# Kernel optimization log

Measured on AMD Instinct MI355X. Metric: run time of the kernel, lower is better.

## Reference

```python
import jax, jax.numpy as jnp
import numpy as np

B, N, K, D = 8, 32768, 128, 64
TAU, ITERS, EPS = 1.0, 10, 1e-8


def setup_inputs() -> dict:
    key = jax.random.key(0)
    k1, k2, k3 = jax.random.split(key, 3)
    xyz = jax.random.normal(k1, (B, 3, N), dtype=jnp.float32)
    feats = jax.random.normal(k2, (B, D, N), dtype=jnp.float32)
    o_scores = jax.random.uniform(k3, (B, N), dtype=jnp.float32)
    return {"xyz": xyz, "feats": feats, "o_scores": o_scores}


def _sq_dist(x, c):
    # x: (B,N,3), c: (B,K,3) -> (B,N,K) squared euclidean distance
    x2 = jnp.sum(x * x, axis=-1, keepdims=True)          # (B,N,1)
    c2 = jnp.sum(c * c, axis=-1)[:, None, :]              # (B,1,K)
    xc = jnp.einsum('bnd,bkd->bnk', x, c)                 # (B,N,K)
    return x2 + c2 - 2.0 * xc


def _wkeans_plus(x, f, s, n_clusters, iters, tau):
    # x: (B,N,3) points, f: (B,N,D) features, s: (B,N) soft weights
    n = x.shape[1]
    # deterministic init: evenly strided points as initial centroids
    init_idx = jnp.arange(n_clusters) * (n // n_clusters)
    centers = x[:, init_idx, :]                           # (B,K,3)
    w = s[..., None]                                      # (B,N,1)
    s_sum = jnp.sum(s, axis=1, keepdims=True) + EPS       # (B,1)
    gamma = None
    denom = None
    for _ in range(iters):
        d = _sq_dist(x, centers)                          # (B,N,K)
        gamma = jax.nn.softmax(-d / tau, axis=-1) * w     # (B,N,K) weighted soft assignment
        denom = jnp.sum(gamma, axis=1) + EPS              # (B,K)
        centers = jnp.einsum('bnk,bnd->bkd', gamma, x) / denom[..., None]
    pi = jnp.sum(gamma, axis=1) / s_sum                   # (B,K) mixing weights
    node_feats = jnp.einsum('bnk,bnd->bkd', gamma, f) / denom[..., None]  # (B,K,D)
    return gamma, pi, centers, node_feats


def reference(xyz, feats, o_scores):
    x = jnp.swapaxes(xyz, -1, -2)    # (B,N,3)
    f = jnp.swapaxes(feats, -1, -2)  # (B,N,D)
    gamma, pi, node_xyz, node_feats = _wkeans_plus(x, f, o_scores, K, ITERS, TAU)
    return gamma, pi, node_xyz, node_feats
```

## Files before the change

kernel.cpp:

```cpp
#include <hip/hip_runtime.h>
#include <hip/hip_bf16.h>

typedef __attribute__((ext_vector_type(8))) short short8;
typedef __attribute__((ext_vector_type(4))) float f32x4;

#define BB 8
#define NN 32768
#define KK 128
#define DD 64
#define TAU 1.0f
#define ITERS 10
#define EPSV 1e-8f
#define JPARTS 128

#define G_SZ   ((size_t)BB * NN * KK)
#define PI_OFF (G_SZ)
#define XY_OFF (PI_OFF + (size_t)BB * KK)
#define NF_OUT (XY_OFF + (size_t)BB * KK * 3)

#define SLICE_F (BB * KK * 4)
#define SS_OFF  ((ITERS + 1) * SLICE_F)
#define HDR_F   (SS_OFF + 16)
#define PART_OFF HDR_F
#define PART_F  ((size_t)JPARTS * BB * KK * DD)
#define WS_NEED_BYTES  ((PART_OFF + PART_F) * 4)

__device__ __forceinline__ unsigned pk2(float a, float b) {
    __hip_bfloat162 h = __float22bfloat162_rn(make_float2(a, b));
    unsigned u; __builtin_memcpy(&u, &h, 4); return u;
}

__global__ __launch_bounds__(256) void prep_kernel(const float* __restrict__ xyz,
                                                   const float* __restrict__ sc,
                                                   float* __restrict__ ws) {
    int b = blockIdx.x, tid = threadIdx.x, wave = tid >> 6, lane = tid & 63;
    const float* S = sc + (size_t)b * NN;
    float sum = 0.f;
    for (int i = tid; i < NN; i += 256) sum += S[i];
    #pragma unroll
    for (int m = 1; m <= 32; m <<= 1) sum += __shfl_xor(sum, m, 64);
    __shared__ float red[4];
    if (lane == 0) red[wave] = sum;
    __syncthreads();
    if (tid == 0) ws[SS_OFF + b] = red[0] + red[1] + red[2] + red[3] + EPSV;
    if (tid < KK) {
        const float* X = xyz + (size_t)b * 3 * NN;
        int i0 = tid * (NN / KK);
        ((float4*)ws)[b * KK + tid] =
            make_float4(X[i0], X[NN + i0], X[2 * NN + i0], 1.0f);
    }
}

template <bool LAST>
__global__ __launch_bounds__(256) void assign_kernel(
    const float* __restrict__ xyz, const float* __restrict__ sc,
    const float4* __restrict__ accIn,
    float* __restrict__ accOut,
    float* __restrict__ gamma_out)
{
    __shared__ float4 cLds[KK];
    __shared__ float4 wLds[512];
    __shared__ float  accW[4][512];

    const int b = blockIdx.y, blk = blockIdx.x;
    const int tid = threadIdx.x, wave = tid >> 6, lane = tid & 63;

    const float* X = xyz + (size_t)b * 3 * NN;
    const float* S = sc + (size_t)b * NN;

    const int n = blk * 512 + tid;
    const float px0 = X[n],       py0 = X[NN + n],       pz0 = X[2 * NN + n],       ps0 = S[n];
    const float px1 = X[n + 256], py1 = X[NN + n + 256], pz1 = X[2 * NN + n + 256], ps1 = S[n + 256];

    if (tid < KK) {
        float4 a = accIn[b * KK + tid];
        float denom = a.w + EPSV;
        float cx = a.x / denom, cy = a.y / denom, cz = a.z / denom;
        cLds[tid] = make_float4(2.f * cx / TAU, 2.f * cy / TAU, 2.f * cz / TAU,
                                -(cx * cx + cy * cy + cz * cz) / TAU);
    }
    __syncthreads();

    float l0a = 0.f, l0b = 0.f, l1a = 0.f, l1b = 0.f;
    #pragma unroll 8
    for (int k = 0; k < KK; k += 2) {
        float4 ca = cLds[k], cb = cLds[k + 1];
        l0a += __expf(fmaf(px0, ca.x, fmaf(py0, ca.y, fmaf(pz0, ca.z, ca.w))));
        l1a += __expf(fmaf(px1, ca.x, fmaf(py1, ca.y, fmaf(pz1, ca.z, ca.w))));
        l0b += __expf(fmaf(px0, cb.x, fmaf(py0, cb.y, fmaf(pz0, cb.z, cb.w))));
        l1b += __expf(fmaf(px1, cb.x, fmaf(py1, cb.y, fmaf(pz1, cb.z, cb.w))));
    }
    wLds[tid]       = make_float4(px0, py0, pz0, ps0 / (l0a + l0b));
    wLds[tid + 256] = make_float4(px1, py1, pz1, ps1 / (l1a + l1b));
    __syncthreads();

    const float4 c0 = cLds[lane];
    const float4 c1 = cLds[lane + 64];
    float ax0 = 0, ay0 = 0, az0 = 0, aw0 = 0;
    float ax1 = 0, ay1 = 0, az1 = 0, aw1 = 0;
    float* grow = gamma_out + ((size_t)b * NN + blk * 512 + (wave << 7)) * KK + lane;

    #pragma unroll 4
    for (int j = 0; j < 128; ++j) {
        float4 P = wLds[(wave << 7) | j];
        float g0 = __expf(fmaf(P.x, c0.x, fmaf(P.y, c0.y, fmaf(P.z, c0.z, c0.w)))) * P.w;
        float g1 = __expf(fmaf(P.x, c1.x, fmaf(P.y, c1.y, fmaf(P.z, c1.z, c1.w)))) * P.w;
        if (LAST) {
            grow[(size_t)j * KK] = g0;
            grow[(size_t)j * KK + 64] = g1;
        }
        ax0 = fmaf(g0, P.x, ax0); ay0 = fmaf(g0, P.y, ay0);
        az0 = fmaf(g0, P.z, az0); aw0 += g0;
        ax1 = fmaf(g1, P.x, ax1); ay1 = fmaf(g1, P.y, ay1);
        az1 = fmaf(g1, P.z, az1); aw1 += g1;
    }

    ((float4*)accW[wave])[lane]      = make_float4(ax0, ay0, az0, aw0);
    ((float4*)accW[wave])[lane + 64] = make_float4(ax1, ay1, az1, aw1);
    __syncthreads();
    float v0 = accW[0][tid]       + accW[1][tid]       + accW[2][tid]       + accW[3][tid];
    float v1 = accW[0][tid + 256] + accW[1][tid + 256] + accW[2][tid + 256] + accW[3][tid + 256];
    float* ag = accOut + b * (KK * 4);
    atomicAdd(ag + tid, v0);
    atomicAdd(ag + tid + 256, v1);
}

__global__ void final_kernel(const float* __restrict__ ws, float* __restrict__ out) {
    int b = blockIdx.x, k = threadIdx.x;
    float4 a = ((const float4*)(ws + ITERS * SLICE_F))[b * KK + k];
    float denom = a.w + EPSV;
    float* oxyz = out + XY_OFF + (size_t)(b * KK + k) * 3;
    oxyz[0] = a.x / denom; oxyz[1] = a.y / denom; oxyz[2] = a.z / denom;
    out[PI_OFF + b * KK + k] = a.w / ws[SS_OFF + b];
}

__global__ __launch_bounds__(256) void nf_mfma2(const float* __restrict__ gamma,
                                                const float* __restrict__ feats,
                                                float* __restrict__ dst) {
    __shared__ unsigned short gT[KK * 40];
    const int b = blockIdx.y, part = blockIdx.x;
    const int tid = threadIdx.x, wave = tid >> 6, lane = tid & 63;
    const int r = lane & 15, hi = lane >> 4;
    const int p = tid & 15, q0 = tid >> 4;

    f32x4 acc[2][4];
    #pragma unroll
    for (int kt = 0; kt < 2; kt++)
        #pragma unroll
        for (int dt = 0; dt < 4; dt++) acc[kt][dt] = (f32x4){0.f, 0.f, 0.f, 0.f};

    const float* gb = gamma + (size_t)b * NN * KK + (size_t)part * 256 * KK;
    const float* fb = feats + (size_t)b * DD * NN;
    const int n0 = part * 256;

    for (int ch = 0; ch < 8; ++ch) {
        const float* gr0 = gb + (size_t)(ch * 32 + 2 * p) * KK;
        const float* gr1 = gr0 + KK;
        unsigned* rowd = (unsigned*)gT;
        #pragma unroll
        for (int s = 0; s < 2; ++s) {
            int q = q0 + 16 * s;
            float4 x = *(const float4*)(gr0 + 4 * q);
            float4 y = *(const float4*)(gr1 + 4 * q);
            rowd[(4 * q + 0) * 20 + p] = pk2(x.x, y.x);
            rowd[(4 * q + 1) * 20 + p] = pk2(x.y, y.y);
            rowd[(4 * q + 2) * 20 + p] = pk2(x.z, y.z);
            rowd[(4 * q + 3) * 20 + p] = pk2(x.w, y.w);
        }
        __syncthreads();

        const unsigned short* a0p = gT + (wave * 32 + r) * 40 + hi * 8;
        short8 a0 = *(const short8*)a0p;
        short8 a1 = *(const short8*)(a0p + 16 * 40);
        const int nn = n0 + ch * 32 + hi * 8;
        #pragma unroll
        for (int dt = 0; dt < 4; ++dt) {
            const float* fr = fb + (size_t)(dt * 16 + r) * NN + nn;
            float4 x = *(const float4*)fr;
            float4 y = *(const float4*)(fr + 4);
            union { unsigned u[4]; short8 s; } bu;
            bu.u[0] = pk2(x.x, x.y); bu.u[1] = pk2(x.z, x.w);
            bu.u[2] = pk2(y.x, y.y); bu.u[3] = pk2(y.z, y.w);
            acc[0][dt] = __builtin_amdgcn_mfma_f32_16x16x32_bf16(a0, bu.s, acc[0][dt], 0, 0, 0);
            acc[1][dt] = __builtin_amdgcn_mfma_f32_16x16x32_bf16(a1, bu.s, acc[1][dt], 0, 0, 0);
        }
        __syncthreads();
    }

    float* pdst = dst + ((size_t)(b * JPARTS + part)) * (KK * DD) + (size_t)(wave * 32) * DD;
    #pragma unroll
    for (int kt = 0; kt < 2; kt++)
        #pragma unroll
        for (int dt = 0; dt < 4; dt++)
            #pragma unroll
            for (int rr = 0; rr < 4; rr++)
                pdst[(kt * 16 + hi * 4 + rr) * DD + dt * 16 + r] = acc[kt][dt][rr];
}

__global__ __launch_bounds__(256) void nf_compute_atomic(const float* __restrict__ gamma,
                                                         const float* __restrict__ feats,
                                                         float* __restrict__ dst) {
    __shared__ float gLds[32 * 128];
    __shared__ float fLds[64 * 33];
    const int b = blockIdx.y, part = blockIdx.x, tid = threadIdx.x;
    const int kq = (tid & 15) * 8, dg = (tid >> 4) * 4;
    float acc[8][4];
    #pragma unroll
    for (int i = 0; i < 8; i++)
        #pragma unroll
        for (int u = 0; u < 4; u++) acc[i][u] = 0.f;
    const float* gb = gamma + (size_t)b * NN * KK + (size_t)part * (NN / JPARTS) * KK;
    const float* fb = feats + (size_t)b * DD * NN + part * (NN / JPARTS);
    for (int ch = 0; ch < (NN / JPARTS) / 32; ++ch) {
        const float4* gs = (const float4*)(gb + (size_t)ch * 32 * KK);
        #pragma unroll
        for (int i = 0; i < 4; i++) ((float4*)gLds)[tid + i * 256] = gs[tid + i * 256];
        #pragma unroll
        for (int i = 0; i < 2; i++) {
            int idx = tid + i * 256;
            int d = idx >> 3, c4 = (idx & 7) * 4;
            float4 fv = *(const float4*)(fb + (size_t)d * NN + ch * 32 + c4);
            float* fr = &fLds[d * 33 + c4];
            fr[0] = fv.x; fr[1] = fv.y; fr[2] = fv.z; fr[3] = fv.w;
        }
        __syncthreads();
        #pragma unroll 4
        for (int nl = 0; nl < 32; ++nl) {
            float4 g0 = *(const float4*)&gLds[nl * 128 + kq];
            float4 g1 = *(const float4*)&gLds[nl * 128 + kq + 4];
            float fv[4];
            #pragma unroll
            for (int u = 0; u < 4; u++) fv[u] = fLds[(dg + u) * 33 + nl];
            float gk[8] = {g0.x, g0.y, g0.z, g0.w, g1.x, g1.y, g1.z, g1.w};
            #pragma unroll
            for (int i = 0; i < 8; i++)
                #pragma unroll
                for (int u = 0; u < 4; u++)
                    acc[i][u] = fmaf(gk[i], fv[u], acc[i][u]);
        }
        __syncthreads();
    }
    float* nf = dst + (size_t)b * KK * DD;
    #pragma unroll
    for (int i = 0; i < 8; i++)
        #pragma unroll
        for (int u = 0; u < 4; u++)
            atomicAdd(&nf[(kq + i) * DD + dg + u], acc[i][u]);
}

__global__ __launch_bounds__(256) void nf_reduce(const float* __restrict__ ws,
                                                 float* __restrict__ out) {
    int idx = blockIdx.x * 256 + threadIdx.x;
    int b = idx >> 13, e = idx & 8191;
    const float* p = ws + PART_OFF + (size_t)b * JPARTS * (KK * DD) + e;
    float sum = 0.f;
    #pragma unroll 8
    for (int j = 0; j < JPARTS; ++j) sum += p[(size_t)j * (KK * DD)];
    int k = e >> 6;
    float denom = ws[ITERS * SLICE_F + (b * KK + k) * 4 + 3] + EPSV;
    out[NF_OUT + idx] = sum / denom;
}

__global__ __launch_bounds__(256) void nf_finalize(const float* __restrict__ ws,
                                                   float* __restrict__ out) {
    int idx = blockIdx.x * 256 + threadIdx.x;
    int bk = idx / DD;
    float denom = ws[ITERS * SLICE_F + bk * 4 + 3] + EPSV;
    out[NF_OUT + idx] = out[NF_OUT + idx] / denom;
}

extern "C" void kernel_launch(void* const* d_in, const int* in_sizes, int n_in,
                              void* d_out, int out_size, void* d_ws, size_t ws_size,
                              hipStream_t stream) {
    const float* xyz = (const float*)d_in[0];
    const float* feats = (const float*)d_in[1];
    const float* sc = (const float*)d_in[2];
    float* out = (float*)d_out;
    float* ws = (float*)d_ws;

    hipMemsetAsync(ws, 0, (size_t)HDR_F * sizeof(float), stream);
    prep_kernel<<<BB, 256, 0, stream>>>(xyz, sc, ws);

    for (int it = 0; it < ITERS - 1; it++) {
        assign_kernel<false><<<dim3(64, BB), 256, 0, stream>>>(
            xyz, sc, (const float4*)(ws + it * SLICE_F),
            ws + (it + 1) * SLICE_F, out);
    }
    assign_kernel<true><<<dim3(64, BB), 256, 0, stream>>>(
        xyz, sc, (const float4*)(ws + (ITERS - 1) * SLICE_F),
        ws + ITERS * SLICE_F, out);

    final_kernel<<<BB, KK, 0, stream>>>(ws, out);

    if (ws_size >= WS_NEED_BYTES) {
        nf_mfma2<<<dim3(JPARTS, BB), 256, 0, stream>>>(out, feats, ws + PART_OFF);
        nf_reduce<<<256, 256, 0, stream>>>(ws, out);
    } else {
        hipMemsetAsync(out + NF_OUT, 0, (size_t)BB * KK * DD * sizeof(float), stream);
        nf_compute_atomic<<<dim3(JPARTS, BB), 256, 0, stream>>>(out, feats, out + NF_OUT);
        nf_finalize<<<256, 256, 0, stream>>>(ws, out);
    }
}
```

Measured before the change: 294.9 us.

## Fuse softmax normalizer into assignment loop via DPP wave reduction

Drops the separate per-point pass that computed the softmax denominator with 128 exponentials per point. The exponentials already computed in the main per-cluster loop are now summed across the wave with a DPP reduction plus readlane, and each value is scaled by the score divided by that sum. Centroids are now held in registers per lane rather than staged through LDS. This roughly halves the exp work, but adds a serial cross-lane reduction chain inside every point iteration.

```diff
diff --git a/kernel.cpp b/kernel.cpp
--- a/kernel.cpp
+++ b/kernel.cpp
@@ -28,6 +28,23 @@
 __device__ __forceinline__ unsigned pk2(float a, float b) {
     __hip_bfloat162 h = __float22bfloat162_rn(make_float2(a, b));
     unsigned u; __builtin_memcpy(&u, &h, 4); return u;
+}
+__device__ __forceinline__ float rdl(float v, int l) {
+    return __int_as_float(__builtin_amdgcn_readlane(__float_as_int(v), l));
+}
+template <int CTRL, int RMASK>
+__device__ __forceinline__ float dpp_add(float x) {
+    int t = __builtin_amdgcn_update_dpp(0, __float_as_int(x), CTRL, RMASK, 0xf, false);
+    return x + __int_as_float(t);
+}
+__device__ __forceinline__ float wave_sum64(float x) {
+    x = dpp_add<0x111, 0xf>(x);
+    x = dpp_add<0x112, 0xf>(x);
+    x = dpp_add<0x114, 0xf>(x);
+    x = dpp_add<0x118, 0xf>(x);
+    x = dpp_add<0x142, 0xa>(x);
+    x = dpp_add<0x143, 0xc>(x);
+    return rdl(x, 63);
 }
 
 __global__ __launch_bounds__(256) void prep_kernel(const float* __restrict__ xyz,
@@ -58,7 +75,6 @@
     float* __restrict__ accOut,
     float* __restrict__ gamma_out)
 {
-    __shared__ float4 cLds[KK];
     __shared__ float4 wLds[512];
     __shared__ float  accW[4][512];
 
@@ -69,33 +85,20 @@
     const float* S = sc + (size_t)b * NN;
 
     const int n = blk * 512 + tid;
-    const float px0 = X[n],       py0 = X[NN + n],       pz0 = X[2 * NN + n],       ps0 = S[n];
-    const float px1 = X[n + 256], py1 = X[NN + n + 256], pz1 = X[2 * NN + n + 256], ps1 = S[n + 256];
-
-    if (tid < KK) {
-        float4 a = accIn[b * KK + tid];
-        float denom = a.w + EPSV;
-        float cx = a.x / denom, cy = a.y / denom, cz = a.z / denom;
-        cLds[tid] = make_float4(2.f * cx / TAU, 2.f * cy / TAU, 2.f * cz / TAU,
-                                -(cx * cx + cy * cy + cz * cz) / TAU);
-    }
+    wLds[tid]       = make_float4(X[n], X[NN + n], X[2 * NN + n], S[n]);
+    wLds[tid + 256] = make_float4(X[n + 256], X[NN + n + 256], X[2 * NN + n + 256], S[n + 256]);
+
+    float4 a0 = accIn[b * KK + lane];
+    float4 a1 = accIn[b * KK + 64 + lane];
+    float d0 = a0.w + EPSV, d1 = a1.w + EPSV;
+    float cx0 = a0.x / d0, cy0 = a0.y / d0, cz0 = a0.z / d0;
+    float cx1 = a1.x / d1, cy1 = a1.y / d1, cz1 = a1.z / d1;
+    const float4 c0 = make_float4(2.f * cx0 / TAU, 2.f * cy0 / TAU, 2.f * cz0 / TAU,
+                                  -(cx0 * cx0 + cy0 * cy0 + cz0 * cz0) / TAU);
+    const float4 c1 = make_float4(2.f * cx1 / TAU, 2.f * cy1 / TAU, 2.f * cz1 / TAU,
+                                  -(cx1 * cx1 + cy1 * cy1 + cz1 * cz1) / TAU);
     __syncthreads();
 
-    float l0a = 0.f, l0b = 0.f, l1a = 0.f, l1b = 0.f;
-    #pragma unroll 8
-    for (int k = 0; k < KK; k += 2) {
-        float4 ca = cLds[k], cb = cLds[k + 1];
-        l0a += __expf(fmaf(px0, ca.x, fmaf(py0, ca.y, fmaf(pz0, ca.z, ca.w))));
-        l1a += __expf(fmaf(px1, ca.x, fmaf(py1, ca.y, fmaf(pz1, ca.z, ca.w))));
-        l0b += __expf(fmaf(px0, cb.x, fmaf(py0, cb.y, fmaf(pz0, cb.z, cb.w))));
-        l1b += __expf(fmaf(px1, cb.x, fmaf(py1, cb.y, fmaf(pz1, cb.z, cb.w))));
-    }
-    wLds[tid]       = make_float4(px0, py0, pz0, ps0 / (l0a + l0b));
-    wLds[tid + 256] = make_float4(px1, py1, pz1, ps1 / (l1a + l1b));
-    __syncthreads();
-
-    const float4 c0 = cLds[lane];
-    const float4 c1 = cLds[lane + 64];
     float ax0 = 0, ay0 = 0, az0 = 0, aw0 = 0;
     float ax1 = 0, ay1 = 0, az1 = 0, aw1 = 0;
     float* grow = gamma_out + ((size_t)b * NN + blk * 512 + (wave << 7)) * KK + lane;
@@ -103,8 +106,11 @@
     #pragma unroll 4
     for (int j = 0; j < 128; ++j) {
         float4 P = wLds[(wave << 7) | j];
-        float g0 = __expf(fmaf(P.x, c0.x, fmaf(P.y, c0.y, fmaf(P.z, c0.z, c0.w)))) * P.w;
-        float g1 = __expf(fmaf(P.x, c1.x, fmaf(P.y, c1.y, fmaf(P.z, c1.z, c1.w)))) * P.w;
+        float e0 = __expf(fmaf(P.x, c0.x, fmaf(P.y, c0.y, fmaf(P.z, c0.z, c0.w))));
+        float e1 = __expf(fmaf(P.x, c1.x, fmaf(P.y, c1.y, fmaf(P.z, c1.z, c1.w))));
+        float l = wave_sum64(e0 + e1);
+        float w = __fdividef(P.w, l);
+        float g0 = e0 * w, g1 = e1 * w;
         if (LAST) {
             grow[(size_t)j * KK] = g0;
             grow[(size_t)j * KK + 64] = g1;
```

After: 322.9 us. +9.5%, slower.

## Fold prep into first assign and final kernels, atomically reduce MFMA node features

Applied to the files above, without the earlier changes.

Removes the separate prep kernel by computing initial centroids inside the first assign launch and moving the score-sum reduction into the final kernel. The MFMA node-feature kernel now atomically adds its partial tiles straight into the output, replacing the per-part workspace partials and the separate reduce pass with a memset plus a light finalize. This cuts launches and the large partial-buffer write and read, at the cost of heavy float atomic contention on a small output.

```diff
diff --git a/kernel.cpp b/kernel.cpp
--- a/kernel.cpp
+++ b/kernel.cpp
@@ -19,39 +19,14 @@
 #define NF_OUT (XY_OFF + (size_t)BB * KK * 3)
 
 #define SLICE_F (BB * KK * 4)
-#define SS_OFF  ((ITERS + 1) * SLICE_F)
-#define HDR_F   (SS_OFF + 16)
-#define PART_OFF HDR_F
-#define PART_F  ((size_t)JPARTS * BB * KK * DD)
-#define WS_NEED_BYTES  ((PART_OFF + PART_F) * 4)
+#define HDR_F   ((ITERS + 1) * SLICE_F)
 
 __device__ __forceinline__ unsigned pk2(float a, float b) {
     __hip_bfloat162 h = __float22bfloat162_rn(make_float2(a, b));
     unsigned u; __builtin_memcpy(&u, &h, 4); return u;
 }
 
-__global__ __launch_bounds__(256) void prep_kernel(const float* __restrict__ xyz,
-                                                   const float* __restrict__ sc,
-                                                   float* __restrict__ ws) {
-    int b = blockIdx.x, tid = threadIdx.x, wave = tid >> 6, lane = tid & 63;
-    const float* S = sc + (size_t)b * NN;
-    float sum = 0.f;
-    for (int i = tid; i < NN; i += 256) sum += S[i];
-    #pragma unroll
-    for (int m = 1; m <= 32; m <<= 1) sum += __shfl_xor(sum, m, 64);
-    __shared__ float red[4];
-    if (lane == 0) red[wave] = sum;
-    __syncthreads();
-    if (tid == 0) ws[SS_OFF + b] = red[0] + red[1] + red[2] + red[3] + EPSV;
-    if (tid < KK) {
-        const float* X = xyz + (size_t)b * 3 * NN;
-        int i0 = tid * (NN / KK);
-        ((float4*)ws)[b * KK + tid] =
-            make_float4(X[i0], X[NN + i0], X[2 * NN + i0], 1.0f);
-    }
-}
-
-template <bool LAST>
+template <bool FIRST, bool LAST>
 __global__ __launch_bounds__(256) void assign_kernel(
     const float* __restrict__ xyz, const float* __restrict__ sc,
     const float4* __restrict__ accIn,
@@ -73,9 +48,15 @@
     const float px1 = X[n + 256], py1 = X[NN + n + 256], pz1 = X[2 * NN + n + 256], ps1 = S[n + 256];
 
     if (tid < KK) {
-        float4 a = accIn[b * KK + tid];
-        float denom = a.w + EPSV;
-        float cx = a.x / denom, cy = a.y / denom, cz = a.z / denom;
+        float cx, cy, cz;
+        if (FIRST) {
+            int i0 = tid * (NN / KK);
+            cx = X[i0]; cy = X[NN + i0]; cz = X[2 * NN + i0];
+        } else {
+            float4 a = accIn[b * KK + tid];
+            float denom = a.w + EPSV;
+            cx = a.x / denom; cy = a.y / denom; cz = a.z / denom;
+        }
         cLds[tid] = make_float4(2.f * cx / TAU, 2.f * cy / TAU, 2.f * cz / TAU,
                                 -(cx * cx + cy * cy + cz * cz) / TAU);
     }
@@ -125,18 +106,31 @@
     atomicAdd(ag + tid + 256, v1);
 }
 
-__global__ void final_kernel(const float* __restrict__ ws, float* __restrict__ out) {
-    int b = blockIdx.x, k = threadIdx.x;
-    float4 a = ((const float4*)(ws + ITERS * SLICE_F))[b * KK + k];
-    float denom = a.w + EPSV;
-    float* oxyz = out + XY_OFF + (size_t)(b * KK + k) * 3;
-    oxyz[0] = a.x / denom; oxyz[1] = a.y / denom; oxyz[2] = a.z / denom;
-    out[PI_OFF + b * KK + k] = a.w / ws[SS_OFF + b];
+__global__ __launch_bounds__(256) void final_kernel(const float* __restrict__ sc,
+                                                    const float* __restrict__ ws,
+                                                    float* __restrict__ out) {
+    int b = blockIdx.x, tid = threadIdx.x, wave = tid >> 6, lane = tid & 63;
+    const float* S = sc + (size_t)b * NN;
+    float sum = 0.f;
+    for (int i = tid; i < NN; i += 256) sum += S[i];
+    #pragma unroll
+    for (int m = 1; m <= 32; m <<= 1) sum += __shfl_xor(sum, m, 64);
+    __shared__ float red[4];
+    if (lane == 0) red[wave] = sum;
+    __syncthreads();
+    if (tid < KK) {
+        float ssum = red[0] + red[1] + red[2] + red[3] + EPSV;
+        float4 a = ((const float4*)(ws + ITERS * SLICE_F))[b * KK + tid];
+        float denom = a.w + EPSV;
+        float* oxyz = out + XY_OFF + (size_t)(b * KK + tid) * 3;
+        oxyz[0] = a.x / denom; oxyz[1] = a.y / denom; oxyz[2] = a.z / denom;
+        out[PI_OFF + b * KK + tid] = a.w / ssum;
+    }
 }
 
 __global__ __launch_bounds__(256) void nf_mfma2(const float* __restrict__ gamma,
                                                 const float* __restrict__ feats,
-                                                float* __restrict__ dst) {
+                                                float* __restrict__ nf_acc) {
     __shared__ unsigned short gT[KK * 40];
     const int b = blockIdx.y, part = blockIdx.x;
     const int tid = threadIdx.x, wave = tid >> 6, lane = tid & 63;
@@ -187,78 +181,15 @@
         __syncthreads();
     }
 
-    float* pdst = dst + ((size_t)(b * JPARTS + part)) * (KK * DD) + (size_t)(wave * 32) * DD;
+    float* nf = nf_acc + (size_t)b * KK * DD + (size_t)(wave * 32) * DD;
     #pragma unroll
     for (int kt = 0; kt < 2; kt++)
         #pragma unroll
         for (int dt = 0; dt < 4; dt++)
             #pragma unroll
             for (int rr = 0; rr < 4; rr++)
-                pdst[(kt * 16 + hi * 4 + rr) * DD + dt * 16 + r] = acc[kt][dt][rr];
-}
-
-__global__ __launch_bounds__(256) void nf_compute_atomic(const float* __restrict__ gamma,
-                                                         const float* __restrict__ feats,
-                                                         float* __restrict__ dst) {
-    __shared__ float gLds[32 * 128];
-    __shared__ float fLds[64 * 33];
-    const int b = blockIdx.y, part = blockIdx.x, tid = threadIdx.x;
-    const int kq = (tid & 15) * 8, dg = (tid >> 4) * 4;
-    float acc[8][4];
-    #pragma unroll
-    for (int i = 0; i < 8; i++)
-        #pragma unroll
-        for (int u = 0; u < 4; u++) acc[i][u] = 0.f;
-    const float* gb = gamma + (size_t)b * NN * KK + (size_t)part * (NN / JPARTS) * KK;
-    const float* fb = feats + (size_t)b * DD * NN + part * (NN / JPARTS);
-    for (int ch = 0; ch < (NN / JPARTS) / 32; ++ch) {
-        const float4* gs = (const float4*)(gb + (size_t)ch * 32 * KK);
-        #pragma unroll
-        for (int i = 0; i < 4; i++) ((float4*)gLds)[tid + i * 256] = gs[tid + i * 256];
-        #pragma unroll
-        for (int i = 0; i < 2; i++) {
-            int idx = tid + i * 256;
-            int d = idx >> 3, c4 = (idx & 7) * 4;
-            float4 fv = *(const float4*)(fb + (size_t)d * NN + ch * 32 + c4);
-            float* fr = &fLds[d * 33 + c4];
-            fr[0] = fv.x; fr[1] = fv.y; fr[2] = fv.z; fr[3] = fv.w;
-        }
-        __syncthreads();
-        #pragma unroll 4
-        for (int nl = 0; nl < 32; ++nl) {
-            float4 g0 = *(const float4*)&gLds[nl * 128 + kq];
-            float4 g1 = *(const float4*)&gLds[nl * 128 + kq + 4];
-            float fv[4];
-            #pragma unroll
-            for (int u = 0; u < 4; u++) fv[u] = fLds[(dg + u) * 33 + nl];
-            float gk[8] = {g0.x, g0.y, g0.z, g0.w, g1.x, g1.y, g1.z, g1.w};
-            #pragma unroll
-            for (int i = 0; i < 8; i++)
-                #pragma unroll
-                for (int u = 0; u < 4; u++)
-                    acc[i][u] = fmaf(gk[i], fv[u], acc[i][u]);
-        }
-        __syncthreads();
-    }
-    float* nf = dst + (size_t)b * KK * DD;
-    #pragma unroll
-    for (int i = 0; i < 8; i++)
-        #pragma unroll
-        for (int u = 0; u < 4; u++)
-            atomicAdd(&nf[(kq + i) * DD + dg + u], acc[i][u]);
-}
-
-__global__ __launch_bounds__(256) void nf_reduce(const float* __restrict__ ws,
-                                                 float* __restrict__ out) {
-    int idx = blockIdx.x * 256 + threadIdx.x;
-    int b = idx >> 13, e = idx & 8191;
-    const float* p = ws + PART_OFF + (size_t)b * JPARTS * (KK * DD) + e;
-    float sum = 0.f;
-    #pragma unroll 8
-    for (int j = 0; j < JPARTS; ++j) sum += p[(size_t)j * (KK * DD)];
-    int k = e >> 6;
-    float denom = ws[ITERS * SLICE_F + (b * KK + k) * 4 + 3] + EPSV;
-    out[NF_OUT + idx] = sum / denom;
+                atomicAdd(&nf[(kt * 16 + hi * 4 + rr) * DD + dt * 16 + r],
+                          acc[kt][dt][rr]);
 }
 
 __global__ __launch_bounds__(256) void nf_finalize(const float* __restrict__ ws,
@@ -279,25 +210,20 @@
     float* ws = (float*)d_ws;
 
     hipMemsetAsync(ws, 0, (size_t)HDR_F * sizeof(float), stream);
-    prep_kernel<<<BB, 256, 0, stream>>>(xyz, sc, ws);
-
-    for (int it = 0; it < ITERS - 1; it++) {
-        assign_kernel<false><<<dim3(64, BB), 256, 0, stream>>>(
+    hipMemsetAsync(out + NF_OUT, 0, (size_t)BB * KK * DD * sizeof(float), stream);
+
+    assign_kernel<true, false><<<dim3(64, BB), 256, 0, stream>>>(
+        xyz, sc, nullptr, ws + SLICE_F, out);
+    for (int it = 1; it < ITERS - 1; it++) {
+        assign_kernel<false, false><<<dim3(64, BB), 256, 0, stream>>>(
             xyz, sc, (const float4*)(ws + it * SLICE_F),
             ws + (it + 1) * SLICE_F, out);
     }
-    assign_kernel<true><<<dim3(64, BB), 256, 0, stream>>>(
+    assign_kernel<false, true><<<dim3(64, BB), 256, 0, stream>>>(
         xyz, sc, (const float4*)(ws + (ITERS - 1) * SLICE_F),
         ws + ITERS * SLICE_F, out);
 
-    final_kernel<<<BB, KK, 0, stream>>>(ws, out);
-
-    if (ws_size >= WS_NEED_BYTES) {
-        nf_mfma2<<<dim3(JPARTS, BB), 256, 0, stream>>>(out, feats, ws + PART_OFF);
-        nf_reduce<<<256, 256, 0, stream>>>(ws, out);
-    } else {
-        hipMemsetAsync(out + NF_OUT, 0, (size_t)BB * KK * DD * sizeof(float), stream);
-        nf_compute_atomic<<<dim3(JPARTS, BB), 256, 0, stream>>>(out, feats, out + NF_OUT);
-        nf_finalize<<<256, 256, 0, stream>>>(ws, out);
-    }
-}
+    final_kernel<<<BB, 256, 0, stream>>>(sc, ws, out);
+    nf_mfma2<<<dim3(JPARTS, BB), 256, 0, stream>>>(out, feats, out + NF_OUT);
+    nf_finalize<<<256, 256, 0, stream>>>(ws, out);
+}
```

Result: no change. 294.8 us (-0.0%).
